# Kernel tuning notes

Hardware: AMD Instinct MI355X
Metric: run time of the kernel (lower is better)

Reference implementation:

```python
import jax, jax.numpy as jnp
import numpy as np

Nx, Nu, Ny, Np, H = 2, 1, 2, 8, 32
Nz = Np * (Nx + Nu)  # 24
B, T = 4096, 256
F, V, Delta = 0.1, 1.0, 1.0  # ps.squeeze(), volume, sample time
ymean = jnp.array([0.5, 0.5], jnp.float32)
ystd = jnp.array([0.3, 0.2], jnp.float32)
umean = jnp.array([1.0], jnp.float32)
ustd = jnp.array([0.5], jnp.float32)


def fnn(x, params):
    # dense layers: tanh hidden, linear output
    for W, b in params[:-1]:
        x = jnp.tanh(x @ W + b)
    W, b = params[-1]
    return x @ W + b


def fxzu(x, z, u, p1, p2, p3):
    # dCa/dt = F*(Caf-Ca)/V - r1 ; dCb/dt = -F*Cb/V + r1 - 3*r2 + r3
    Castd, Cbstd = ystd[0:1], ystd[1:2]
    r1 = fnn(x[:, 0:1], p1) * Castd
    r2 = fnn(x[:, 1:2], p2) * Cbstd
    r3 = fnn(z, p3) * Cbstd
    xs = x * ystd + ymean
    us = u * ustd + umean
    Ca, Cb, Caf = xs[:, 0:1], xs[:, 1:2], us[:, 0:1]
    dCa = F * (Caf - Ca) / V - r1
    dCb = -F * Cb / V + r1 - 3.0 * r2 + r3
    return jnp.concatenate([dCa, dCb], axis=-1) / ystd


def interp(yseq):
    # (B,(Np+1)*Nx) -> (B, Np*Nx): midpoints of consecutive Nx-blocks
    b = yseq.shape[0]
    y = yseq.reshape(b, Np + 1, Nx)
    return (0.5 * (y[:, :-1] + y[:, 1:])).reshape(b, Np * Nx)


def run(useq, xz0, p1, p2, p3):
    def step(xz, u):
        x, z = xz[:, :Nx], xz[:, Nx:]
        xpseq, upseq = z[:, :Np * Nx], z[:, Np * Nx:]
        k1 = fxzu(x, z, u, p1, p2, p3)
        z23 = jnp.concatenate([interp(jnp.concatenate([xpseq, x], -1)), upseq], -1)
        k2 = fxzu(x + Delta * k1 / 2, z23, u, p1, p2, p3)
        k3 = fxzu(x + Delta * k2 / 2, z23, u, p1, p2, p3)
        z4 = jnp.concatenate([xpseq[:, Nx:], x, upseq], -1)
        k4 = fxzu(x + Delta * k3, z4, u, p1, p2, p3)
        xplus = x + (Delta / 6.0) * (k1 + 2 * k2 + 2 * k3 + k4)
        zplus = jnp.concatenate([xpseq[:, Nx:], x, upseq[:, Nu:], u], -1)
        return jnp.concatenate([xplus, zplus], -1), x  # output is pre-update x
    _, ys = jax.lax.scan(step, xz0, jnp.swapaxes(useq, 0, 1))
    return jnp.swapaxes(ys, 0, 1)  # (B, T, Ny)


def setup_inputs() -> dict:
    key = jax.random.key(0)
    ks = jax.random.split(key, 12)
    inp = {
        'useq': jax.random.normal(ks[0], (B, T, Nu), jnp.float32),
        'xz0': jax.random.normal(ks[1], (B, Nx + Nz), jnp.float32),
    }
    dims = {'r1': [1, H, H, 1], 'r2': [1, H, H, 1], 'r3': [Nz, H, H, 1]}
    i = 2
    for name, ds in dims.items():
        for l, (din, dout) in enumerate(zip(ds[:-1], ds[1:])):
            inp[f'{name}W{l}'] = jax.random.normal(ks[i], (din, dout), jnp.float32) / np.sqrt(din).astype(np.float32)
            inp[f'{name}b{l}'] = jnp.zeros((dout,), jnp.float32)
            i += 1
    return inp


def reference(useq, xz0, r1W0, r1b0, r1W1, r1b1, r1W2, r1b2,
              r2W0, r2b0, r2W1, r2b1, r2W2, r2b2,
              r3W0, r3b0, r3W1, r3b1, r3W2, r3b2):
    p1 = [(r1W0, r1b0), (r1W1, r1b1), (r1W2, r1b2)]
    p2 = [(r2W0, r2b0), (r2W1, r2b1), (r2W2, r2b2)]
    p3 = [(r3W0, r3b0), (r3W1, r3b1), (r3W2, r3b2)]
    return run(useq, xz0, p1, p2, p3)
```

## Files before the change

kernel.cpp:

```cpp
#include <hip/hip_runtime.h>

#define DEVINL static __device__ __forceinline__
#define CFENCE() asm volatile("" ::: "memory")

typedef float v2f __attribute__((ext_vector_type(2)));

DEVINL v2f mk2(float a, float b) { v2f r; r.x = a; r.y = b; return r; }
DEVINL v2f pkfma(v2f a, v2f b, v2f c) { return __builtin_elementwise_fma(a, b, c); }

constexpr float KE = 2.885390081777927f;

#if __has_builtin(__builtin_amdgcn_exp2f)
DEVINL float exp2_fast(float x) { return __builtin_amdgcn_exp2f(x); }
#else
DEVINL float exp2_fast(float x) { return __expf(x * 0.6931471805599453f); }
#endif

DEVINL float tanh_pre(float t) {
  float e = exp2_fast(t);
  return 1.0f - 2.0f * __builtin_amdgcn_rcpf(e + 1.0f);
}

template <int CTRL>
DEVINL float dpp_add(float v) {
  int t = __builtin_amdgcn_update_dpp(0, __float_as_int(v), CTRL, 0xF, 0xF, true);
  return v + __int_as_float(t);
}
DEVINL float halves_total(float v) {
  v = dpp_add<0xB1>(v);
  v = dpp_add<0x4E>(v);
  v = dpp_add<0x141>(v);
  v = dpp_add<0x140>(v);
  v = dpp_add<0x142>(v);
  return v;
}
DEVINL float rlane(float v, int l) {
  return __int_as_float(__builtin_amdgcn_readlane(__float_as_int(v), l));
}

DEVINL float dot32(const float* hrow, const v2f* W, float bias) {
  const float4* hp = (const float4*)hrow;
  v2f a0 = mk2(bias, 0.f), a1 = mk2(0.f, 0.f);
  v2f a2 = mk2(0.f, 0.f), a3 = mk2(0.f, 0.f);
#pragma unroll
  for (int q = 0; q < 8; q += 2) {
    float4 x = hp[q], y = hp[q + 1];
    a0 = pkfma(mk2(x.x, x.y), W[2 * q + 0], a0);
    a1 = pkfma(mk2(x.z, x.w), W[2 * q + 1], a1);
    a2 = pkfma(mk2(y.x, y.y), W[2 * q + 2], a2);
    a3 = pkfma(mk2(y.z, y.w), W[2 * q + 3], a3);
  }
  v2f s = (a0 + a1) + (a2 + a3);
  return s.x + s.y;
}
DEVINL float pdot16(const float* hrow, const v2f* W) {
  const float4* hp = (const float4*)hrow;
  v2f a0 = mk2(0.f, 0.f), a1 = mk2(0.f, 0.f);
  float4 x = hp[0], y = hp[1];
  a0 = pkfma(mk2(x.x, x.y), W[0], a0);
  a1 = pkfma(mk2(x.z, x.w), W[1], a1);
  a0 = pkfma(mk2(y.x, y.y), W[2], a0);
  a1 = pkfma(mk2(y.z, y.w), W[3], a1);
  x = hp[2]; y = hp[3];
  a0 = pkfma(mk2(x.x, x.y), W[4], a0);
  a1 = pkfma(mk2(x.z, x.w), W[5], a1);
  a0 = pkfma(mk2(y.x, y.y), W[6], a0);
  a1 = pkfma(mk2(y.z, y.w), W[7], a1);
  v2f s = a0 + a1;
  return s.x + s.y;
}

constexpr int TT = 256;

__global__ __attribute__((amdgpu_flat_work_group_size(64, 64)))
__attribute__((amdgpu_waves_per_eu(4, 4))) void reac_kernel(
    const float* __restrict__ useq,
    const float* __restrict__ xz0,
    const float* __restrict__ r1W0, const float* __restrict__ r1b0,
    const float* __restrict__ r1W1, const float* __restrict__ r1b1,
    const float* __restrict__ r1W2, const float* __restrict__ r1b2,
    const float* __restrict__ r2W0, const float* __restrict__ r2b0,
    const float* __restrict__ r2W1, const float* __restrict__ r2b1,
    const float* __restrict__ r2W2, const float* __restrict__ r2b2,
    const float* __restrict__ r3W0, const float* __restrict__ r3b0,
    const float* __restrict__ r3W1, const float* __restrict__ r3b1,
    const float* __restrict__ r3W2, const float* __restrict__ r3b2,
    float2* __restrict__ out)
{
  const int lane = threadIdx.x;
  const int j = lane & 31;
  const bool hi = lane >= 32;
  const int b = blockIdx.x;
  const int xaddr = ((lane ^ 32) << 2);

  auto xchg = [&](float v) -> float {
    return __int_as_float(__builtin_amdgcn_ds_bpermute(xaddr, __float_as_int(v)));
  };

  const float* W0p = hi ? r2W0 : r1W0;
  const float* B0p = hi ? r2b0 : r1b0;
  const float* W1p = hi ? r2W1 : r1W1;
  const float* B1p = hi ? r2b1 : r1b1;
  const float* W2p = hi ? r2W2 : r1W2;
  const float sc = hi ? 0.2f : 0.3f;
  float w0K = W0p[j] * KE, b0K = B0p[j] * KE;
  float b1K = B1p[j] * KE;
  float w2sc = W2p[j] * sc;

  v2f W1v[16];
#pragma unroll
  for (int k = 0; k < 16; ++k)
    W1v[k] = mk2(W1p[(2 * k) * 32 + j] * KE, W1p[(2 * k + 1) * 32 + j] * KE);

  v2f W0Cv[12];
#pragma unroll
  for (int m = 0; m < 12; ++m)
    W0Cv[m] = mk2(r3W0[(2 * m) * 32 + j] * KE, r3W0[(2 * m + 1) * 32 + j] * KE);
  const int kbase = hi ? 16 : 0;
  v2f W1Cv[8];
#pragma unroll
  for (int k = 0; k < 8; ++k)
    W1Cv[k] = mk2(r3W1[(kbase + 2 * k) * 32 + j] * KE,
                  r3W1[(kbase + 2 * k + 1) * 32 + j] * KE);
  float b0CK = r3b0[j] * KE, b1CK = r3b1[j] * KE;
  float w2C02 = r3W2[j] * 0.2f;

  const float b2sA = r1b2[0] * 0.3f;
  const float b2sB = r2b2[0] * 0.2f;
  const float b2Cs = r3b2[0] * 0.2f - 0.05f;

  __shared__ __align__(16) float zs[24];
  __shared__ __align__(16) float zb[16];
  __shared__ __align__(16) float h12[2][32];
  __shared__ __align__(16) float hR3[3][32];

  float x0 = xz0[b * 26 + 0];
  float x1 = xz0[b * 26 + 1];
  if (!hi && j < 24) zs[j] = xz0[b * 26 + 2 + j];
  CFENCE();

  auto stage = [&](float sxv, float syv, float rc_m05, float CafF,
                   float& kx, float& ky) {
    float sv = hi ? syv : sxv;
    float h = tanh_pre(fmaf(sv, w0K, b0K));
    CFENCE();
    h12[hi][j] = h;
    CFENCE();
    float a = dot32(&h12[hi][0], W1v, b1K);
    float v = halves_total(tanh_pre(a) * w2sc);
    float ra = rlane(v, 31) + b2sA;
    float rb = rlane(v, 63) + b2sB;
    float dCa = fmaf(-0.03f, sxv, CafF) - ra;
    float dCb = fmaf(-0.02f, syv, fmaf(-3.0f, rb, ra) + rc_m05);
    kx = dCa * (1.0f / 0.3f);
    ky = dCb * (1.0f / 0.2f);
  };

  float u = useq[b * TT];

  for (int t = 0; t < TT; ++t) {
    int tn = (t < TT - 1) ? (t + 1) : t;
    float u_nxt = useq[b * TT + tn];
    float CafF = fmaf(u, 0.05f, 0.05f);

    if (lane == 0) out[b * TT + t] = make_float2(x0, x1);

    CFENCE();
    if (!hi && j < 16) {
      zb[j] = (j < 14) ? zs[j + 2] : ((j == 14) ? x0 : x1);
    }
    CFENCE();

    const float4* zp = (const float4*)(hi ? &zb[0] : &zs[0]);
    float4 z0 = zp[0], z1 = zp[1], z2 = zp[2], z3 = zp[3];
    const float4* up = (const float4*)&zs[16];
    float4 u0 = up[0], u1 = up[1];
    v2f aa = mk2(b0CK, 0.f), ab = mk2(0.f, 0.f);
    aa = pkfma(mk2(z0.x, z0.y), W0Cv[0], aa);
    ab = pkfma(mk2(z0.z, z0.w), W0Cv[1], ab);
    aa = pkfma(mk2(z1.x, z1.y), W0Cv[2], aa);
    ab = pkfma(mk2(z1.z, z1.w), W0Cv[3], ab);
    aa = pkfma(mk2(z2.x, z2.y), W0Cv[4], aa);
    ab = pkfma(mk2(z2.z, z2.w), W0Cv[5], ab);
    aa = pkfma(mk2(z3.x, z3.y), W0Cv[6], aa);
    ab = pkfma(mk2(z3.z, z3.w), W0Cv[7], ab);
    aa = pkfma(mk2(u0.x, u0.y), W0Cv[8], aa);
    ab = pkfma(mk2(u0.z, u0.w), W0Cv[9], ab);
    aa = pkfma(mk2(u1.x, u1.y), W0Cv[10], aa);
    ab = pkfma(mk2(u1.z, u1.w), W0Cv[11], ab);
    v2f as = aa + ab;
    float A = as.x + as.y;
    float Ap = xchg(A);
    float tA = tanh_pre(A);
    CFENCE();
    if (!hi) {
      hR3[0][j] = tA;
      hR3[1][j] = tanh_pre(0.5f * (A + Ap));
    } else {
      hR3[2][j] = tA;
    }
    CFENCE();
    float p0 = pdot16(&hR3[0][kbase], W1Cv);
    float p1 = pdot16(&hR3[1][kbase], W1Cv);
    float p2 = pdot16(&hR3[2][kbase], W1Cv);
    float o0 = p0 + xchg(p0) + b1CK;
    float o1 = p1 + xchg(p1) + b1CK;
    float o2 = p2 + xchg(p2) + b1CK;
    float v0 = halves_total(tanh_pre(o0) * w2C02);
    float v1 = halves_total(tanh_pre(o1) * w2C02);
    float v2 = halves_total(tanh_pre(o2) * w2C02);
    float rc1  = rlane(v0, 31) + b2Cs;
    float rc23 = rlane(v1, 31) + b2Cs;
    float rc4  = rlane(v2, 31) + b2Cs;

    float kx1, ky1, kx2, ky2, kx3, ky3, kx4, ky4;
    stage(x0, x1, rc1, CafF, kx1, ky1);
    stage(fmaf(kx1, 0.5f, x0), fmaf(ky1, 0.5f, x1), rc23, CafF, kx2, ky2);
    stage(fmaf(kx2, 0.5f, x0), fmaf(ky2, 0.5f, x1), rc23, CafF, kx3, ky3);
    stage(x0 + kx3, x1 + ky3, rc4, CafF, kx4, ky4);

    float znew = 0.0f;
    bool updz = (!hi) && (j < 24);
    if (updz) znew = (j < 16) ? zb[j] : ((j < 23) ? zs[j + 1] : u);
    CFENCE();
    if (updz) zs[j] = znew;
    x0 += (kx1 + 2.0f * (kx2 + kx3) + kx4) * (1.0f / 6.0f);
    x1 += (ky1 + 2.0f * (ky2 + ky3) + ky4) * (1.0f / 6.0f);
    u = u_nxt;
    CFENCE();
  }
}

extern "C" void kernel_launch(void* const* d_in, const int* in_sizes, int n_in,
                              void* d_out, int out_size, void* d_ws, size_t ws_size,
                              hipStream_t stream) {
  const float* p[20];
  for (int i = 0; i < 20; ++i) p[i] = (const float*)d_in[i];
  reac_kernel<<<dim3(4096), dim3(64), 0, stream>>>(
      p[0], p[1], p[2], p[3], p[4], p[5], p[6], p[7], p[8], p[9], p[10],
      p[11], p[12], p[13], p[14], p[15], p[16], p[17], p[18], p[19],
      (float2*)d_out);
}
```

Before: 850.6 us.

## Software-pipeline r3 network across steps and fold z-shift into weights

Restructures the per-step schedule so the z-dependent part of the r3 first layer and the rc1 evaluation for the next step are computed during the current step's RK stages. The shifted z4 input is handled by permuting the upper-half weights and adding x-dependent terms via a separate weight pair, which removes the zb shared buffer and one layer-two evaluation per step. It also adds a block-index-dependent s_sleep at start to stagger wave phases. The cost is more complex LDS ordering, and it relies on wavefront-level implicit synchronisation between the shared-memory writes and reads.

```diff
diff --git a/kernel.cpp b/kernel.cpp
--- a/kernel.cpp
+++ b/kernel.cpp
@@ -93,6 +93,12 @@
   const int b = blockIdx.x;
   const int xaddr = ((lane ^ 32) << 2);
 
+  {
+    int phase = (b >> 8) & 3;
+    if (phase & 1) __builtin_amdgcn_s_sleep(2);
+    if (phase & 2) __builtin_amdgcn_s_sleep(4);
+  }
+
   auto xchg = [&](float v) -> float {
     return __int_as_float(__builtin_amdgcn_ds_bpermute(xaddr, __float_as_int(v)));
   };
@@ -114,8 +120,14 @@
 
   v2f W0Cv[12];
 #pragma unroll
-  for (int m = 0; m < 12; ++m)
-    W0Cv[m] = mk2(r3W0[(2 * m) * 32 + j] * KE, r3W0[(2 * m + 1) * 32 + j] * KE);
+  for (int m = 0; m < 12; ++m) {
+    int r = (hi && m >= 1 && m <= 7) ? (2 * m - 2) : (2 * m);
+    v2f w = mk2(r3W0[r * 32 + j] * KE, r3W0[(r + 1) * 32 + j] * KE);
+    if (hi && m == 0) w = mk2(0.f, 0.f);
+    W0Cv[m] = w;
+  }
+  const v2f WXv = mk2(r3W0[14 * 32 + j] * KE, r3W0[15 * 32 + j] * KE);
+
   const int kbase = hi ? 16 : 0;
   v2f W1Cv[8];
 #pragma unroll
@@ -130,7 +142,6 @@
   const float b2Cs = r3b2[0] * 0.2f - 0.05f;
 
   __shared__ __align__(16) float zs[24];
-  __shared__ __align__(16) float zb[16];
   __shared__ __align__(16) float h12[2][32];
   __shared__ __align__(16) float hR3[3][32];
 
@@ -139,13 +150,37 @@
   if (!hi && j < 24) zs[j] = xz0[b * 26 + 2 + j];
   CFENCE();
 
-  auto stage = [&](float sxv, float syv, float rc_m05, float CafF,
-                   float& kx, float& ky) {
+  auto r3_l0 = [&](v2f& aaO, v2f& abO) {
+    const float4* zp4 = (const float4*)&zs[0];
+    float4 z0v = zp4[0], z1v = zp4[1], z2v = zp4[2], z3v = zp4[3];
+    float4 u0v = zp4[4], u1v = zp4[5];
+    v2f aa = mk2(b0CK, 0.f), ab = mk2(0.f, 0.f);
+    aa = pkfma(mk2(z0v.x, z0v.y), W0Cv[0], aa);
+    ab = pkfma(mk2(z0v.z, z0v.w), W0Cv[1], ab);
+    aa = pkfma(mk2(z1v.x, z1v.y), W0Cv[2], aa);
+    ab = pkfma(mk2(z1v.z, z1v.w), W0Cv[3], ab);
+    aa = pkfma(mk2(z2v.x, z2v.y), W0Cv[4], aa);
+    ab = pkfma(mk2(z2v.z, z2v.w), W0Cv[5], ab);
+    aa = pkfma(mk2(z3v.x, z3v.y), W0Cv[6], aa);
+    ab = pkfma(mk2(z3v.z, z3v.w), W0Cv[7], ab);
+    aa = pkfma(mk2(u0v.x, u0v.y), W0Cv[8], aa);
+    ab = pkfma(mk2(u0v.z, u0v.w), W0Cv[9], ab);
+    aa = pkfma(mk2(u1v.x, u1v.y), W0Cv[10], aa);
+    ab = pkfma(mk2(u1v.z, u1v.w), W0Cv[11], ab);
+    aaO = aa; abO = ab;
+  };
+  auto rc1_eval = [&]() -> float {
+    float p0 = pdot16(&hR3[0][kbase], W1Cv);
+    float o0 = p0 + xchg(p0) + b1CK;
+    return rlane(halves_total(tanh_pre(o0) * w2C02), 31) + b2Cs;
+  };
+
+  auto net_pre = [&](float sxv, float syv) -> float {
     float sv = hi ? syv : sxv;
-    float h = tanh_pre(fmaf(sv, w0K, b0K));
-    CFENCE();
-    h12[hi][j] = h;
-    CFENCE();
+    return tanh_pre(fmaf(sv, w0K, b0K));
+  };
+  auto net_post = [&](float sxv, float syv, float rc_m05, float CafF,
+                      float& kx, float& ky) {
     float a = dot32(&h12[hi][0], W1v, b1K);
     float v = halves_total(tanh_pre(a) * w2sc);
     float ra = rlane(v, 31) + b2sA;
@@ -156,6 +191,19 @@
     ky = dCb * (1.0f / 0.2f);
   };
 
+  v2f aa4, ab4;
+  float Az;
+  r3_l0(aa4, ab4);
+  {
+    v2f s = aa4 + ab4;
+    Az = s.x + s.y;
+    float h0 = tanh_pre(Az);
+    CFENCE();
+    if (!hi) hR3[0][j] = h0;
+    CFENCE();
+  }
+  float rc1 = rc1_eval();
+
   float u = useq[b * TT];
 
   for (int t = 0; t < TT; ++t) {
@@ -165,65 +213,62 @@
 
     if (lane == 0) out[b * TT + t] = make_float2(x0, x1);
 
-    CFENCE();
-    if (!hi && j < 16) {
-      zb[j] = (j < 14) ? zs[j + 2] : ((j == 14) ? x0 : x1);
-    }
-    CFENCE();
-
-    const float4* zp = (const float4*)(hi ? &zb[0] : &zs[0]);
-    float4 z0 = zp[0], z1 = zp[1], z2 = zp[2], z3 = zp[3];
-    const float4* up = (const float4*)&zs[16];
-    float4 u0 = up[0], u1 = up[1];
-    v2f aa = mk2(b0CK, 0.f), ab = mk2(0.f, 0.f);
-    aa = pkfma(mk2(z0.x, z0.y), W0Cv[0], aa);
-    ab = pkfma(mk2(z0.z, z0.w), W0Cv[1], ab);
-    aa = pkfma(mk2(z1.x, z1.y), W0Cv[2], aa);
-    ab = pkfma(mk2(z1.z, z1.w), W0Cv[3], ab);
-    aa = pkfma(mk2(z2.x, z2.y), W0Cv[4], aa);
-    ab = pkfma(mk2(z2.z, z2.w), W0Cv[5], ab);
-    aa = pkfma(mk2(z3.x, z3.y), W0Cv[6], aa);
-    ab = pkfma(mk2(z3.z, z3.w), W0Cv[7], ab);
-    aa = pkfma(mk2(u0.x, u0.y), W0Cv[8], aa);
-    ab = pkfma(mk2(u0.z, u0.w), W0Cv[9], ab);
-    aa = pkfma(mk2(u1.x, u1.y), W0Cv[10], aa);
-    ab = pkfma(mk2(u1.z, u1.w), W0Cv[11], ab);
-    v2f as = aa + ab;
-    float A = as.x + as.y;
-    float Ap = xchg(A);
-    float tA = tanh_pre(A);
-    CFENCE();
-    if (!hi) {
-      hR3[0][j] = tA;
-      hR3[1][j] = tanh_pre(0.5f * (A + Ap));
-    } else {
-      hR3[2][j] = tA;
-    }
-    CFENCE();
-    float p0 = pdot16(&hR3[0][kbase], W1Cv);
+    ab4 = pkfma(mk2(x0, x1), WXv, ab4);
+    v2f s4v = aa4 + ab4;
+    float A4 = s4v.x + s4v.y;
+    float Apart = xchg(hi ? A4 : Az);
+    float targ = hi ? A4 : (0.5f * (Az + Apart));
+    float hh = tanh_pre(targ);
+    float h1 = net_pre(x0, x1);
+    CFENCE();
+    hR3[1 + hi][j] = hh;
+    h12[hi][j] = h1;
+    CFENCE();
     float p1 = pdot16(&hR3[1][kbase], W1Cv);
     float p2 = pdot16(&hR3[2][kbase], W1Cv);
-    float o0 = p0 + xchg(p0) + b1CK;
     float o1 = p1 + xchg(p1) + b1CK;
     float o2 = p2 + xchg(p2) + b1CK;
-    float v0 = halves_total(tanh_pre(o0) * w2C02);
-    float v1 = halves_total(tanh_pre(o1) * w2C02);
-    float v2 = halves_total(tanh_pre(o2) * w2C02);
-    float rc1  = rlane(v0, 31) + b2Cs;
-    float rc23 = rlane(v1, 31) + b2Cs;
-    float rc4  = rlane(v2, 31) + b2Cs;
-
-    float kx1, ky1, kx2, ky2, kx3, ky3, kx4, ky4;
-    stage(x0, x1, rc1, CafF, kx1, ky1);
-    stage(fmaf(kx1, 0.5f, x0), fmaf(ky1, 0.5f, x1), rc23, CafF, kx2, ky2);
-    stage(fmaf(kx2, 0.5f, x0), fmaf(ky2, 0.5f, x1), rc23, CafF, kx3, ky3);
-    stage(x0 + kx3, x1 + ky3, rc4, CafF, kx4, ky4);
-
-    float znew = 0.0f;
-    bool updz = (!hi) && (j < 24);
-    if (updz) znew = (j < 16) ? zb[j] : ((j < 23) ? zs[j + 1] : u);
-    CFENCE();
-    if (updz) zs[j] = znew;
+    float vv = halves_total(tanh_pre(hi ? o2 : o1) * w2C02);
+    float rc23 = rlane(vv, 31) + b2Cs;
+    float rc4  = rlane(vv, 63) + b2Cs;
+    float kx1, ky1;
+    net_post(x0, x1, rc1, CafF, kx1, ky1);
+    float sx2 = fmaf(kx1, 0.5f, x0), sy2 = fmaf(ky1, 0.5f, x1);
+    float h2 = net_pre(sx2, sy2);
+    CFENCE();
+    h12[hi][j] = h2;
+    CFENCE();
+    float kx2, ky2;
+    net_post(sx2, sy2, rc23, CafF, kx2, ky2);
+    {
+      int src = (j < 14) ? (j + 2) : ((j < 23) ? (j + 1) : 0);
+      float zread = zs[src];
+      float znew = (j == 14) ? x0 : ((j == 15) ? x1 : ((j == 23) ? u : zread));
+      if ((!hi) && (j < 24)) zs[j] = znew;
+    }
+    CFENCE();
+    r3_l0(aa4, ab4);
+    {
+      v2f sv2 = aa4 + ab4;
+      Az = sv2.x + sv2.y;
+      float h0n = tanh_pre(Az);
+      if (!hi) hR3[0][j] = h0n;
+    }
+    float sx3 = fmaf(kx2, 0.5f, x0), sy3 = fmaf(ky2, 0.5f, x1);
+    float h3 = net_pre(sx3, sy3);
+    CFENCE();
+    h12[hi][j] = h3;
+    CFENCE();
+    float kx3, ky3;
+    net_post(sx3, sy3, rc23, CafF, kx3, ky3);
+    rc1 = rc1_eval();
+    float sx4 = x0 + kx3, sy4 = x1 + ky3;
+    float h4 = net_pre(sx4, sy4);
+    CFENCE();
+    h12[hi][j] = h4;
+    CFENCE();
+    float kx4, ky4;
+    net_post(sx4, sy4, rc4, CafF, kx4, ky4);
     x0 += (kx1 + 2.0f * (kx2 + kx3) + kx4) * (1.0f / 6.0f);
     x1 += (ky1 + 2.0f * (ky2 + ky3) + ky4) * (1.0f / 6.0f);
     u = u_nxt;
```

Result: faster. 790.4 us (-7.1%).

## Map one batch element per half-wave and software-pipeline r3 layer-0 across steps

Applied to the files above, without the earlier changes.

Each 32-lane half-wave now handles a whole batch element: it holds both r1 and r2 weights plus the full r3 W1, and grid size is halved. The r3 first layer is split so the x-dependent term is added incrementally. The next step's z-part is computed early, overlapping with stage 3/4, and reductions use a DPP plus ds_swizzle within 32 lanes. This removes cross-half exchanges and readlane broadcasts, at the cost of more registers (waves_per_eu lowered to 2) and more serial work per lane.

```diff
diff --git a/kernel.cpp b/kernel.cpp
--- a/kernel.cpp
+++ b/kernel.cpp
@@ -26,16 +26,13 @@
   int t = __builtin_amdgcn_update_dpp(0, __float_as_int(v), CTRL, 0xF, 0xF, true);
   return v + __int_as_float(t);
 }
-DEVINL float halves_total(float v) {
+DEVINL float elem_total(float v) {
   v = dpp_add<0xB1>(v);
   v = dpp_add<0x4E>(v);
   v = dpp_add<0x141>(v);
   v = dpp_add<0x140>(v);
-  v = dpp_add<0x142>(v);
-  return v;
-}
-DEVINL float rlane(float v, int l) {
-  return __int_as_float(__builtin_amdgcn_readlane(__float_as_int(v), l));
+  int s = __builtin_amdgcn_ds_swizzle(__float_as_int(v), 0x401F);
+  return v + __int_as_float(s);
 }
 
 DEVINL float dot32(const float* hrow, const v2f* W, float bias) {
@@ -53,27 +50,11 @@
   v2f s = (a0 + a1) + (a2 + a3);
   return s.x + s.y;
 }
-DEVINL float pdot16(const float* hrow, const v2f* W) {
-  const float4* hp = (const float4*)hrow;
-  v2f a0 = mk2(0.f, 0.f), a1 = mk2(0.f, 0.f);
-  float4 x = hp[0], y = hp[1];
-  a0 = pkfma(mk2(x.x, x.y), W[0], a0);
-  a1 = pkfma(mk2(x.z, x.w), W[1], a1);
-  a0 = pkfma(mk2(y.x, y.y), W[2], a0);
-  a1 = pkfma(mk2(y.z, y.w), W[3], a1);
-  x = hp[2]; y = hp[3];
-  a0 = pkfma(mk2(x.x, x.y), W[4], a0);
-  a1 = pkfma(mk2(x.z, x.w), W[5], a1);
-  a0 = pkfma(mk2(y.x, y.y), W[6], a0);
-  a1 = pkfma(mk2(y.z, y.w), W[7], a1);
-  v2f s = a0 + a1;
-  return s.x + s.y;
-}
 
 constexpr int TT = 256;
 
 __global__ __attribute__((amdgpu_flat_work_group_size(64, 64)))
-__attribute__((amdgpu_waves_per_eu(4, 4))) void reac_kernel(
+__attribute__((amdgpu_waves_per_eu(2, 2))) void reac_kernel(
     const float* __restrict__ useq,
     const float* __restrict__ xz0,
     const float* __restrict__ r1W0, const float* __restrict__ r1b0,
@@ -91,37 +72,33 @@
   const int j = lane & 31;
   const bool hi = lane >= 32;
   const int b = blockIdx.x;
-  const int xaddr = ((lane ^ 32) << 2);
-
-  auto xchg = [&](float v) -> float {
-    return __int_as_float(__builtin_amdgcn_ds_bpermute(xaddr, __float_as_int(v)));
-  };
-
-  const float* W0p = hi ? r2W0 : r1W0;
-  const float* B0p = hi ? r2b0 : r1b0;
-  const float* W1p = hi ? r2W1 : r1W1;
-  const float* B1p = hi ? r2b1 : r1b1;
-  const float* W2p = hi ? r2W2 : r1W2;
-  const float sc = hi ? 0.2f : 0.3f;
-  float w0K = W0p[j] * KE, b0K = B0p[j] * KE;
-  float b1K = B1p[j] * KE;
-  float w2sc = W2p[j] * sc;
-
-  v2f W1v[16];
+  const int ge = 2 * b + (hi ? 1 : 0);
+
+  float w0K1 = r1W0[j] * KE, b0K1 = r1b0[j] * KE;
+  float w0K2 = r2W0[j] * KE, b0K2 = r2b0[j] * KE;
+  float b1K1 = r1b1[j] * KE, b1K2 = r2b1[j] * KE;
+  float w2s1 = r1W2[j] * 0.3f, w2s2 = r2W2[j] * 0.2f;
+
+  v2f W1a[16], W1b[16];
+#pragma unroll
+  for (int k = 0; k < 16; ++k) {
+    W1a[k] = mk2(r1W1[(2 * k) * 32 + j] * KE, r1W1[(2 * k + 1) * 32 + j] * KE);
+    W1b[k] = mk2(r2W1[(2 * k) * 32 + j] * KE, r2W1[(2 * k + 1) * 32 + j] * KE);
+  }
+
+  v2f WZ[8], WU[4];
+#pragma unroll
+  for (int m = 0; m < 8; ++m)
+    WZ[m] = mk2(r3W0[(2 * m) * 32 + j] * KE, r3W0[(2 * m + 1) * 32 + j] * KE);
+#pragma unroll
+  for (int m = 0; m < 4; ++m)
+    WU[m] = mk2(r3W0[(16 + 2 * m) * 32 + j] * KE,
+                r3W0[(17 + 2 * m) * 32 + j] * KE);
+
+  v2f W1C[16];
 #pragma unroll
   for (int k = 0; k < 16; ++k)
-    W1v[k] = mk2(W1p[(2 * k) * 32 + j] * KE, W1p[(2 * k + 1) * 32 + j] * KE);
-
-  v2f W0Cv[12];
-#pragma unroll
-  for (int m = 0; m < 12; ++m)
-    W0Cv[m] = mk2(r3W0[(2 * m) * 32 + j] * KE, r3W0[(2 * m + 1) * 32 + j] * KE);
-  const int kbase = hi ? 16 : 0;
-  v2f W1Cv[8];
-#pragma unroll
-  for (int k = 0; k < 8; ++k)
-    W1Cv[k] = mk2(r3W1[(kbase + 2 * k) * 32 + j] * KE,
-                  r3W1[(kbase + 2 * k + 1) * 32 + j] * KE);
+    W1C[k] = mk2(r3W1[(2 * k) * 32 + j] * KE, r3W1[(2 * k + 1) * 32 + j] * KE);
   float b0CK = r3b0[j] * KE, b1CK = r3b1[j] * KE;
   float w2C02 = r3W2[j] * 0.2f;
 
@@ -129,103 +106,155 @@
   const float b2sB = r2b2[0] * 0.2f;
   const float b2Cs = r3b2[0] * 0.2f - 0.05f;
 
-  __shared__ __align__(16) float zs[24];
-  __shared__ __align__(16) float zb[16];
-  __shared__ __align__(16) float h12[2][32];
-  __shared__ __align__(16) float hR3[3][32];
-
-  float x0 = xz0[b * 26 + 0];
-  float x1 = xz0[b * 26 + 1];
-  if (!hi && j < 24) zs[j] = xz0[b * 26 + 2 + j];
+  __shared__ __align__(16) float zs2[2][24];
+  __shared__ __align__(16) float h12s[2][2][32];
+  __shared__ __align__(16) float hR3s[2][3][32];
+
+  float* zse  = &zs2[hi ? 1 : 0][0];
+  float* h12a = &h12s[hi ? 1 : 0][0][0];
+  float* h12b = h12a + 32;
+  float* hR3e = &hR3s[hi ? 1 : 0][0][0];
+
+  float x0 = xz0[ge * 26 + 0];
+  float x1 = xz0[ge * 26 + 1];
+  if (j < 24) zse[j] = xz0[ge * 26 + 2 + j];
   CFENCE();
 
-  auto stage = [&](float sxv, float syv, float rc_m05, float CafF,
-                   float& kx, float& ky) {
-    float sv = hi ? syv : sxv;
-    float h = tanh_pre(fmaf(sv, w0K, b0K));
-    CFENCE();
-    h12[hi][j] = h;
-    CFENCE();
-    float a = dot32(&h12[hi][0], W1v, b1K);
-    float v = halves_total(tanh_pre(a) * w2sc);
-    float ra = rlane(v, 31) + b2sA;
-    float rb = rlane(v, 63) + b2sB;
-    float dCa = fmaf(-0.03f, sxv, CafF) - ra;
-    float dCb = fmaf(-0.02f, syv, fmaf(-3.0f, rb, ra) + rc_m05);
+  auto r3_l0 = [&](float& AzO, float& A4pO) {
+    const float4* zp = (const float4*)zse;
+    float4 z0v = zp[0], z1v = zp[1], z2v = zp[2], z3v = zp[3];
+    float4 u0v = zp[4], u1v = zp[5];
+    v2f pa = mk2(b0CK, 0.f), pb = mk2(0.f, 0.f);
+    pa = pkfma(mk2(z0v.x, z0v.y), WZ[0], pa);
+    pb = pkfma(mk2(z0v.z, z0v.w), WZ[1], pb);
+    pa = pkfma(mk2(z1v.x, z1v.y), WZ[2], pa);
+    pb = pkfma(mk2(z1v.z, z1v.w), WZ[3], pb);
+    pa = pkfma(mk2(z2v.x, z2v.y), WZ[4], pa);
+    pb = pkfma(mk2(z2v.z, z2v.w), WZ[5], pb);
+    pa = pkfma(mk2(z3v.x, z3v.y), WZ[6], pa);
+    pb = pkfma(mk2(z3v.z, z3v.w), WZ[7], pb);
+    pa = pkfma(mk2(u0v.x, u0v.y), WU[0], pa);
+    pb = pkfma(mk2(u0v.z, u0v.w), WU[1], pb);
+    pa = pkfma(mk2(u1v.x, u1v.y), WU[2], pa);
+    pb = pkfma(mk2(u1v.z, u1v.w), WU[3], pb);
+    v2f s = pa + pb;
+    AzO = s.x + s.y;
+    v2f qa = mk2(b0CK, 0.f), qb = mk2(0.f, 0.f);
+    qa = pkfma(mk2(z0v.z, z0v.w), WZ[0], qa);
+    qb = pkfma(mk2(z1v.x, z1v.y), WZ[1], qb);
+    qa = pkfma(mk2(z1v.z, z1v.w), WZ[2], qa);
+    qb = pkfma(mk2(z2v.x, z2v.y), WZ[3], qb);
+    qa = pkfma(mk2(z2v.z, z2v.w), WZ[4], qa);
+    qb = pkfma(mk2(z3v.x, z3v.y), WZ[5], qb);
+    qa = pkfma(mk2(z3v.z, z3v.w), WZ[6], qa);
+    qb = pkfma(mk2(u0v.x, u0v.y), WU[0], qb);
+    qa = pkfma(mk2(u0v.z, u0v.w), WU[1], qa);
+    qb = pkfma(mk2(u1v.x, u1v.y), WU[2], qb);
+    qa = pkfma(mk2(u1v.z, u1v.w), WU[3], qa);
+    v2f s2 = qa + qb;
+    A4pO = s2.x + s2.y;
+  };
+
+  auto stage_finish = [&](float a1, float a2, float sx, float sy, float rc,
+                          float CafF, float& kx, float& ky) {
+    float ra = elem_total(tanh_pre(a1) * w2s1) + b2sA;
+    float rb = elem_total(tanh_pre(a2) * w2s2) + b2sB;
+    float dCa = fmaf(-0.03f, sx, CafF) - ra;
+    float dCb = fmaf(-0.02f, sy, fmaf(-3.0f, rb, ra) + rc);
     kx = dCa * (1.0f / 0.3f);
     ky = dCb * (1.0f / 0.2f);
   };
 
-  float u = useq[b * TT];
+  float Az, A4p;
+  r3_l0(Az, A4p);
+  {
+    float h0 = tanh_pre(Az);
+    CFENCE();
+    hR3e[j] = h0;
+    CFENCE();
+  }
+  float o0 = dot32(hR3e, W1C, b1CK);
+  float rc1 = elem_total(tanh_pre(o0) * w2C02) + b2Cs;
+
+  const float* up = useq + ge * TT;
+  float2* outp = out + ge * TT;
+  float u = up[0];
 
   for (int t = 0; t < TT; ++t) {
     int tn = (t < TT - 1) ? (t + 1) : t;
-    float u_nxt = useq[b * TT + tn];
+    float u_nxt = up[tn];
     float CafF = fmaf(u, 0.05f, 0.05f);
 
-    if (lane == 0) out[b * TT + t] = make_float2(x0, x1);
-
-    CFENCE();
-    if (!hi && j < 16) {
-      zb[j] = (j < 14) ? zs[j + 2] : ((j == 14) ? x0 : x1);
-    }
-    CFENCE();
-
-    const float4* zp = (const float4*)(hi ? &zb[0] : &zs[0]);
-    float4 z0 = zp[0], z1 = zp[1], z2 = zp[2], z3 = zp[3];
-    const float4* up = (const float4*)&zs[16];
-    float4 u0 = up[0], u1 = up[1];
-    v2f aa = mk2(b0CK, 0.f), ab = mk2(0.f, 0.f);
-    aa = pkfma(mk2(z0.x, z0.y), W0Cv[0], aa);
-    ab = pkfma(mk2(z0.z, z0.w), W0Cv[1], ab);
-    aa = pkfma(mk2(z1.x, z1.y), W0Cv[2], aa);
-    ab = pkfma(mk2(z1.z, z1.w), W0Cv[3], ab);
-    aa = pkfma(mk2(z2.x, z2.y), W0Cv[4], aa);
-    ab = pkfma(mk2(z2.z, z2.w), W0Cv[5], ab);
-    aa = pkfma(mk2(z3.x, z3.y), W0Cv[6], aa);
-    ab = pkfma(mk2(z3.z, z3.w), W0Cv[7], ab);
-    aa = pkfma(mk2(u0.x, u0.y), W0Cv[8], aa);
-    ab = pkfma(mk2(u0.z, u0.w), W0Cv[9], ab);
-    aa = pkfma(mk2(u1.x, u1.y), W0Cv[10], aa);
-    ab = pkfma(mk2(u1.z, u1.w), W0Cv[11], ab);
-    v2f as = aa + ab;
-    float A = as.x + as.y;
-    float Ap = xchg(A);
-    float tA = tanh_pre(A);
-    CFENCE();
-    if (!hi) {
-      hR3[0][j] = tA;
-      hR3[1][j] = tanh_pre(0.5f * (A + Ap));
-    } else {
-      hR3[2][j] = tA;
-    }
-    CFENCE();
-    float p0 = pdot16(&hR3[0][kbase], W1Cv);
-    float p1 = pdot16(&hR3[1][kbase], W1Cv);
-    float p2 = pdot16(&hR3[2][kbase], W1Cv);
-    float o0 = p0 + xchg(p0) + b1CK;
-    float o1 = p1 + xchg(p1) + b1CK;
-    float o2 = p2 + xchg(p2) + b1CK;
-    float v0 = halves_total(tanh_pre(o0) * w2C02);
-    float v1 = halves_total(tanh_pre(o1) * w2C02);
-    float v2 = halves_total(tanh_pre(o2) * w2C02);
-    float rc1  = rlane(v0, 31) + b2Cs;
-    float rc23 = rlane(v1, 31) + b2Cs;
-    float rc4  = rlane(v2, 31) + b2Cs;
-
-    float kx1, ky1, kx2, ky2, kx3, ky3, kx4, ky4;
-    stage(x0, x1, rc1, CafF, kx1, ky1);
-    stage(fmaf(kx1, 0.5f, x0), fmaf(ky1, 0.5f, x1), rc23, CafF, kx2, ky2);
-    stage(fmaf(kx2, 0.5f, x0), fmaf(ky2, 0.5f, x1), rc23, CafF, kx3, ky3);
-    stage(x0 + kx3, x1 + ky3, rc4, CafF, kx4, ky4);
-
-    float znew = 0.0f;
-    bool updz = (!hi) && (j < 24);
-    if (updz) znew = (j < 16) ? zb[j] : ((j < 23) ? zs[j + 1] : u);
-    CFENCE();
-    if (updz) zs[j] = znew;
+    if (j == 0) outp[t] = make_float2(x0, x1);
+
+    float A4 = fmaf(x1, WZ[7].y, fmaf(x0, WZ[7].x, A4p));
+    float A23 = 0.5f * (Az + A4);
+    float h23 = tanh_pre(A23);
+    float h4v = tanh_pre(A4);
+    float g1a = tanh_pre(fmaf(x0, w0K1, b0K1));
+    float g1b = tanh_pre(fmaf(x1, w0K2, b0K2));
+    CFENCE();
+    hR3e[32 + j] = h23;
+    hR3e[64 + j] = h4v;
+    h12a[j] = g1a;
+    h12b[j] = g1b;
+    CFENCE();
+    float o1 = dot32(hR3e + 32, W1C, b1CK);
+    float o2 = dot32(hR3e + 64, W1C, b1CK);
+    float a1 = dot32(h12a, W1a, b1K1);
+    float a2 = dot32(h12b, W1b, b1K2);
+    float rc23 = elem_total(tanh_pre(o1) * w2C02) + b2Cs;
+    float rc4  = elem_total(tanh_pre(o2) * w2C02) + b2Cs;
+    float kx1, ky1;
+    stage_finish(a1, a2, x0, x1, rc1, CafF, kx1, ky1);
+    float sx2 = fmaf(kx1, 0.5f, x0), sy2 = fmaf(ky1, 0.5f, x1);
+    float g2a = tanh_pre(fmaf(sx2, w0K1, b0K1));
+    float g2b = tanh_pre(fmaf(sy2, w0K2, b0K2));
+    CFENCE();
+    h12a[j] = g2a;
+    h12b[j] = g2b;
+    CFENCE();
+    float a1_2 = dot32(h12a, W1a, b1K1);
+    float a2_2 = dot32(h12b, W1b, b1K2);
+    int src = (j < 14) ? (j + 2) : ((j < 23) ? (j + 1) : 0);
+    float zread = zse[src];
+    float kx2, ky2;
+    stage_finish(a1_2, a2_2, sx2, sy2, rc23, CafF, kx2, ky2);
+    float znew = (j == 14) ? x0 : ((j == 15) ? x1 : ((j == 23) ? u : zread));
+    CFENCE();
+    if (j < 24) zse[j] = znew;
+    float sx3 = fmaf(kx2, 0.5f, x0), sy3 = fmaf(ky2, 0.5f, x1);
+    float g3a = tanh_pre(fmaf(sx3, w0K1, b0K1));
+    float g3b = tanh_pre(fmaf(sy3, w0K2, b0K2));
+    CFENCE();
+    h12a[j] = g3a;
+    h12b[j] = g3b;
+    CFENCE();
+    float a1_3 = dot32(h12a, W1a, b1K1);
+    float a2_3 = dot32(h12b, W1b, b1K2);
+    float Azn, A4pn;
+    r3_l0(Azn, A4pn);
+    float kx3, ky3;
+    stage_finish(a1_3, a2_3, sx3, sy3, rc23, CafF, kx3, ky3);
+    float sx4 = x0 + kx3, sy4 = x1 + ky3;
+    float g4a = tanh_pre(fmaf(sx4, w0K1, b0K1));
+    float g4b = tanh_pre(fmaf(sy4, w0K2, b0K2));
+    float h0n = tanh_pre(Azn);
+    CFENCE();
+    h12a[j] = g4a;
+    h12b[j] = g4b;
+    hR3e[j] = h0n;
+    CFENCE();
+    float a1_4 = dot32(h12a, W1a, b1K1);
+    float a2_4 = dot32(h12b, W1b, b1K2);
+    float o0n = dot32(hR3e, W1C, b1CK);
+    float kx4, ky4;
+    stage_finish(a1_4, a2_4, sx4, sy4, rc4, CafF, kx4, ky4);
+    rc1 = elem_total(tanh_pre(o0n) * w2C02) + b2Cs;
     x0 += (kx1 + 2.0f * (kx2 + kx3) + kx4) * (1.0f / 6.0f);
     x1 += (ky1 + 2.0f * (ky2 + ky3) + ky4) * (1.0f / 6.0f);
+    Az = Azn;
+    A4p = A4pn;
     u = u_nxt;
     CFENCE();
   }
@@ -236,7 +265,7 @@
                               hipStream_t stream) {
   const float* p[20];
   for (int i = 0; i < 20; ++i) p[i] = (const float*)d_in[i];
-  reac_kernel<<<dim3(4096), dim3(64), 0, stream>>>(
+  reac_kernel<<<dim3(2048), dim3(64), 0, stream>>>(
       p[0], p[1], p[2], p[3], p[4], p[5], p[6], p[7], p[8], p[9], p[10],
       p[11], p[12], p[13], p[14], p[15], p[16], p[17], p[18], p[19],
       (float2*)d_out);
```

Measured after the change: 803.6 us. -5.5%, faster.

## Process two batch elements per wave with interleaved, software-pipelined RK4 stages

Applied to the files above, without the earlier changes.

Each 64-lane wave now handles two batch rows, interleaving their independent dependency chains to expose more instruction-level parallelism in the latency-bound serial scan. The r3 first layer is restructured so the z4 variant reuses partial accumulators plus an x-only update, and the next step's rc1 network is computed early, overlapping with stage 3. The DPP reduction is shortened to 16-lane groups combined via readlane. Grid halves and waves_per_eu drops to 2, trading occupancy for more registers and ILP.

```diff
diff --git a/kernel.cpp b/kernel.cpp
--- a/kernel.cpp
+++ b/kernel.cpp
@@ -26,16 +26,15 @@
   int t = __builtin_amdgcn_update_dpp(0, __float_as_int(v), CTRL, 0xF, 0xF, true);
   return v + __int_as_float(t);
 }
-DEVINL float halves_total(float v) {
+DEVINL float rlane(float v, int l) {
+  return __int_as_float(__builtin_amdgcn_readlane(__float_as_int(v), l));
+}
+DEVINL float psum4(float v) {
   v = dpp_add<0xB1>(v);
   v = dpp_add<0x4E>(v);
   v = dpp_add<0x141>(v);
   v = dpp_add<0x140>(v);
-  v = dpp_add<0x142>(v);
   return v;
-}
-DEVINL float rlane(float v, int l) {
-  return __int_as_float(__builtin_amdgcn_readlane(__float_as_int(v), l));
 }
 
 DEVINL float dot32(const float* hrow, const v2f* W, float bias) {
@@ -73,7 +72,7 @@
 constexpr int TT = 256;
 
 __global__ __attribute__((amdgpu_flat_work_group_size(64, 64)))
-__attribute__((amdgpu_waves_per_eu(4, 4))) void reac_kernel(
+__attribute__((amdgpu_waves_per_eu(2, 2))) void reac_kernel(
     const float* __restrict__ useq,
     const float* __restrict__ xz0,
     const float* __restrict__ r1W0, const float* __restrict__ r1b0,
@@ -114,8 +113,14 @@
 
   v2f W0Cv[12];
 #pragma unroll
-  for (int m = 0; m < 12; ++m)
-    W0Cv[m] = mk2(r3W0[(2 * m) * 32 + j] * KE, r3W0[(2 * m + 1) * 32 + j] * KE);
+  for (int m = 0; m < 12; ++m) {
+    int r = (hi && m >= 1 && m <= 7) ? (2 * m - 2) : (2 * m);
+    v2f w = mk2(r3W0[r * 32 + j] * KE, r3W0[(r + 1) * 32 + j] * KE);
+    if (hi && m == 0) w = mk2(0.f, 0.f);
+    W0Cv[m] = w;
+  }
+  v2f WXv = mk2(r3W0[14 * 32 + j] * KE, r3W0[15 * 32 + j] * KE);
+
   const int kbase = hi ? 16 : 0;
   v2f W1Cv[8];
 #pragma unroll
@@ -129,52 +134,31 @@
   const float b2sB = r2b2[0] * 0.2f;
   const float b2Cs = r3b2[0] * 0.2f - 0.05f;
 
-  __shared__ __align__(16) float zs[24];
-  __shared__ __align__(16) float zb[16];
-  __shared__ __align__(16) float h12[2][32];
-  __shared__ __align__(16) float hR3[3][32];
-
-  float x0 = xz0[b * 26 + 0];
-  float x1 = xz0[b * 26 + 1];
-  if (!hi && j < 24) zs[j] = xz0[b * 26 + 2 + j];
+  __shared__ __align__(16) float zsS[2][24];
+  __shared__ __align__(16) float h12S[2][2][32];
+  __shared__ __align__(16) float hR3S[2][3][32];
+
+  struct Elem {
+    float x0, x1, Az, rc1, u;
+    v2f aa4, ab4;
+    float* zs; float* h12; float* hR3;
+    const float* up; float2* outp;
+  } EA, EB;
+  EA.zs = &zsS[0][0]; EA.h12 = &h12S[0][0][0]; EA.hR3 = &hR3S[0][0][0];
+  EB.zs = &zsS[1][0]; EB.h12 = &h12S[1][0][0]; EB.hR3 = &hR3S[1][0][0];
+  EA.up = useq + (2 * b + 0) * TT; EA.outp = out + (2 * b + 0) * TT;
+  EB.up = useq + (2 * b + 1) * TT; EB.outp = out + (2 * b + 1) * TT;
+
+  EA.x0 = xz0[(2 * b + 0) * 26 + 0]; EA.x1 = xz0[(2 * b + 0) * 26 + 1];
+  EB.x0 = xz0[(2 * b + 1) * 26 + 0]; EB.x1 = xz0[(2 * b + 1) * 26 + 1];
+  if (!hi && j < 24) EA.zs[j] = xz0[(2 * b + 0) * 26 + 2 + j];
+  if (hi && j < 24)  EB.zs[j] = xz0[(2 * b + 1) * 26 + 2 + j];
   CFENCE();
 
-  auto stage = [&](float sxv, float syv, float rc_m05, float CafF,
-                   float& kx, float& ky) {
-    float sv = hi ? syv : sxv;
-    float h = tanh_pre(fmaf(sv, w0K, b0K));
-    CFENCE();
-    h12[hi][j] = h;
-    CFENCE();
-    float a = dot32(&h12[hi][0], W1v, b1K);
-    float v = halves_total(tanh_pre(a) * w2sc);
-    float ra = rlane(v, 31) + b2sA;
-    float rb = rlane(v, 63) + b2sB;
-    float dCa = fmaf(-0.03f, sxv, CafF) - ra;
-    float dCb = fmaf(-0.02f, syv, fmaf(-3.0f, rb, ra) + rc_m05);
-    kx = dCa * (1.0f / 0.3f);
-    ky = dCb * (1.0f / 0.2f);
-  };
-
-  float u = useq[b * TT];
-
-  for (int t = 0; t < TT; ++t) {
-    int tn = (t < TT - 1) ? (t + 1) : t;
-    float u_nxt = useq[b * TT + tn];
-    float CafF = fmaf(u, 0.05f, 0.05f);
-
-    if (lane == 0) out[b * TT + t] = make_float2(x0, x1);
-
-    CFENCE();
-    if (!hi && j < 16) {
-      zb[j] = (j < 14) ? zs[j + 2] : ((j == 14) ? x0 : x1);
-    }
-    CFENCE();
-
-    const float4* zp = (const float4*)(hi ? &zb[0] : &zs[0]);
+  auto r3_l0 = [&](Elem& E) {
+    const float4* zp = (const float4*)E.zs;
     float4 z0 = zp[0], z1 = zp[1], z2 = zp[2], z3 = zp[3];
-    const float4* up = (const float4*)&zs[16];
-    float4 u0 = up[0], u1 = up[1];
+    float4 u0 = zp[4], u1 = zp[5];
     v2f aa = mk2(b0CK, 0.f), ab = mk2(0.f, 0.f);
     aa = pkfma(mk2(z0.x, z0.y), W0Cv[0], aa);
     ab = pkfma(mk2(z0.z, z0.w), W0Cv[1], ab);
@@ -188,45 +172,152 @@
     ab = pkfma(mk2(u0.z, u0.w), W0Cv[9], ab);
     aa = pkfma(mk2(u1.x, u1.y), W0Cv[10], aa);
     ab = pkfma(mk2(u1.z, u1.w), W0Cv[11], ab);
-    v2f as = aa + ab;
-    float A = as.x + as.y;
-    float Ap = xchg(A);
-    float tA = tanh_pre(A);
-    CFENCE();
-    if (!hi) {
-      hR3[0][j] = tA;
-      hR3[1][j] = tanh_pre(0.5f * (A + Ap));
-    } else {
-      hR3[2][j] = tA;
+    E.aa4 = aa; E.ab4 = ab;
+    v2f s = aa + ab;
+    E.Az = s.x + s.y;
+  };
+  auto rc1_eval = [&](Elem& E) -> float {
+    float p0 = pdot16(&E.hR3[kbase], W1Cv);
+    float o0 = p0 + xchg(p0) + b1CK;
+    float v = psum4(tanh_pre(o0) * w2C02);
+    return (rlane(v, 15) + rlane(v, 31)) + b2Cs;
+  };
+  auto net_pre = [&](float sxv, float syv) -> float {
+    float sv = hi ? syv : sxv;
+    return tanh_pre(fmaf(sv, w0K, b0K));
+  };
+  auto net_post = [&](Elem& E, float sxv, float syv, float rc_m05,
+                      float CafF, float& kx, float& ky) {
+    float a = dot32(&E.h12[hi ? 32 : 0], W1v, b1K);
+    float v = psum4(tanh_pre(a) * w2sc);
+    float ra = (rlane(v, 15) + rlane(v, 31)) + b2sA;
+    float rb = (rlane(v, 47) + rlane(v, 63)) + b2sB;
+    float dCa = fmaf(-0.03f, sxv, CafF) - ra;
+    float dCb = fmaf(-0.02f, syv, fmaf(-3.0f, rb, ra) + rc_m05);
+    kx = dCa * (1.0f / 0.3f);
+    ky = dCb * (1.0f / 0.2f);
+  };
+
+  r3_l0(EA);
+  r3_l0(EB);
+  {
+    float h0A = tanh_pre(EA.Az);
+    float h0B = tanh_pre(EB.Az);
+    CFENCE();
+    if (!hi) { EA.hR3[j] = h0A; EB.hR3[j] = h0B; }
+    CFENCE();
+  }
+  EA.rc1 = rc1_eval(EA);
+  EB.rc1 = rc1_eval(EB);
+  EA.u = EA.up[0];
+  EB.u = EB.up[0];
+
+  for (int t = 0; t < TT; ++t) {
+    int tn = (t < TT - 1) ? (t + 1) : t;
+    float uAn = EA.up[tn], uBn = EB.up[tn];
+    float CafFA = fmaf(EA.u, 0.05f, 0.05f);
+    float CafFB = fmaf(EB.u, 0.05f, 0.05f);
+
+    {
+      float2 val = hi ? make_float2(EB.x0, EB.x1) : make_float2(EA.x0, EA.x1);
+      float2* addr = hi ? EB.outp : EA.outp;
+      if (j == 0) addr[t] = val;
     }
-    CFENCE();
-    float p0 = pdot16(&hR3[0][kbase], W1Cv);
-    float p1 = pdot16(&hR3[1][kbase], W1Cv);
-    float p2 = pdot16(&hR3[2][kbase], W1Cv);
-    float o0 = p0 + xchg(p0) + b1CK;
-    float o1 = p1 + xchg(p1) + b1CK;
-    float o2 = p2 + xchg(p2) + b1CK;
-    float v0 = halves_total(tanh_pre(o0) * w2C02);
-    float v1 = halves_total(tanh_pre(o1) * w2C02);
-    float v2 = halves_total(tanh_pre(o2) * w2C02);
-    float rc1  = rlane(v0, 31) + b2Cs;
-    float rc23 = rlane(v1, 31) + b2Cs;
-    float rc4  = rlane(v2, 31) + b2Cs;
-
-    float kx1, ky1, kx2, ky2, kx3, ky3, kx4, ky4;
-    stage(x0, x1, rc1, CafF, kx1, ky1);
-    stage(fmaf(kx1, 0.5f, x0), fmaf(ky1, 0.5f, x1), rc23, CafF, kx2, ky2);
-    stage(fmaf(kx2, 0.5f, x0), fmaf(ky2, 0.5f, x1), rc23, CafF, kx3, ky3);
-    stage(x0 + kx3, x1 + ky3, rc4, CafF, kx4, ky4);
-
-    float znew = 0.0f;
-    bool updz = (!hi) && (j < 24);
-    if (updz) znew = (j < 16) ? zb[j] : ((j < 23) ? zs[j + 1] : u);
-    CFENCE();
-    if (updz) zs[j] = znew;
-    x0 += (kx1 + 2.0f * (kx2 + kx3) + kx4) * (1.0f / 6.0f);
-    x1 += (ky1 + 2.0f * (ky2 + ky3) + ky4) * (1.0f / 6.0f);
-    u = u_nxt;
+
+    EA.ab4 = pkfma(mk2(EA.x0, EA.x1), WXv, EA.ab4);
+    EB.ab4 = pkfma(mk2(EB.x0, EB.x1), WXv, EB.ab4);
+    v2f s4A = EA.aa4 + EA.ab4;
+    v2f s4B = EB.aa4 + EB.ab4;
+    float A4A = s4A.x + s4A.y;
+    float A4B = s4B.x + s4B.y;
+    float ApA = xchg(hi ? A4A : EA.Az);
+    float ApB = xchg(hi ? A4B : EB.Az);
+    float tgA = hi ? A4A : (0.5f * (EA.Az + ApA));
+    float tgB = hi ? A4B : (0.5f * (EB.Az + ApB));
+    float hhA = tanh_pre(tgA);
+    float hhB = tanh_pre(tgB);
+    float h1A = net_pre(EA.x0, EA.x1);
+    float h1B = net_pre(EB.x0, EB.x1);
+    CFENCE();
+    EA.hR3[32 * (1 + (hi ? 1 : 0)) + j] = hhA;
+    EB.hR3[32 * (1 + (hi ? 1 : 0)) + j] = hhB;
+    EA.h12[(hi ? 32 : 0) + j] = h1A;
+    EB.h12[(hi ? 32 : 0) + j] = h1B;
+    CFENCE();
+    float p1A = pdot16(&EA.hR3[32 + kbase], W1Cv);
+    float p2A = pdot16(&EA.hR3[64 + kbase], W1Cv);
+    float p1B = pdot16(&EB.hR3[32 + kbase], W1Cv);
+    float p2B = pdot16(&EB.hR3[64 + kbase], W1Cv);
+    float o1A = p1A + xchg(p1A) + b1CK;
+    float o2A = p2A + xchg(p2A) + b1CK;
+    float o1B = p1B + xchg(p1B) + b1CK;
+    float o2B = p2B + xchg(p2B) + b1CK;
+    float vvA = psum4(tanh_pre(hi ? o2A : o1A) * w2C02);
+    float vvB = psum4(tanh_pre(hi ? o2B : o1B) * w2C02);
+    float rc23A = (rlane(vvA, 15) + rlane(vvA, 31)) + b2Cs;
+    float rc4A  = (rlane(vvA, 47) + rlane(vvA, 63)) + b2Cs;
+    float rc23B = (rlane(vvB, 15) + rlane(vvB, 31)) + b2Cs;
+    float rc4B  = (rlane(vvB, 47) + rlane(vvB, 63)) + b2Cs;
+    float kx1A, ky1A, kx1B, ky1B;
+    net_post(EA, EA.x0, EA.x1, EA.rc1, CafFA, kx1A, ky1A);
+    net_post(EB, EB.x0, EB.x1, EB.rc1, CafFB, kx1B, ky1B);
+    float sx2A = fmaf(kx1A, 0.5f, EA.x0), sy2A = fmaf(ky1A, 0.5f, EA.x1);
+    float sx2B = fmaf(kx1B, 0.5f, EB.x0), sy2B = fmaf(ky1B, 0.5f, EB.x1);
+    float h2A = net_pre(sx2A, sy2A);
+    float h2B = net_pre(sx2B, sy2B);
+    CFENCE();
+    EA.h12[(hi ? 32 : 0) + j] = h2A;
+    EB.h12[(hi ? 32 : 0) + j] = h2B;
+    CFENCE();
+    float kx2A, ky2A, kx2B, ky2B;
+    net_post(EA, sx2A, sy2A, rc23A, CafFA, kx2A, ky2A);
+    net_post(EB, sx2B, sy2B, rc23B, CafFB, kx2B, ky2B);
+    int src = (j < 14) ? (j + 2) : ((j < 23) ? (j + 1) : 0);
+    float zrA = EA.zs[src];
+    float zrB = EB.zs[src];
+    float znA = (j == 14) ? EA.x0
+              : ((j == 15) ? EA.x1 : ((j == 23) ? EA.u : zrA));
+    float znB = (j == 14) ? EB.x0
+              : ((j == 15) ? EB.x1 : ((j == 23) ? EB.u : zrB));
+    CFENCE();
+    if (!hi && j < 24) EA.zs[j] = znA;
+    if (hi && j < 24)  EB.zs[j] = znB;
+    float sx3A = fmaf(kx2A, 0.5f, EA.x0), sy3A = fmaf(ky2A, 0.5f, EA.x1);
+    float sx3B = fmaf(kx2B, 0.5f, EB.x0), sy3B = fmaf(ky2B, 0.5f, EB.x1);
+    float h3A = net_pre(sx3A, sy3A);
+    float h3B = net_pre(sx3B, sy3B);
+    CFENCE();
+    r3_l0(EA);
+    r3_l0(EB);
+    float h0nA = tanh_pre(EA.Az);
+    float h0nB = tanh_pre(EB.Az);
+    if (!hi) { EA.hR3[j] = h0nA; EB.hR3[j] = h0nB; }
+    CFENCE();
+    EA.h12[(hi ? 32 : 0) + j] = h3A;
+    EB.h12[(hi ? 32 : 0) + j] = h3B;
+    CFENCE();
+    float kx3A, ky3A, kx3B, ky3B;
+    net_post(EA, sx3A, sy3A, rc23A, CafFA, kx3A, ky3A);
+    net_post(EB, sx3B, sy3B, rc23B, CafFB, kx3B, ky3B);
+    float rc1An = rc1_eval(EA);
+    float rc1Bn = rc1_eval(EB);
+    float sx4A = EA.x0 + kx3A, sy4A = EA.x1 + ky3A;
+    float sx4B = EB.x0 + kx3B, sy4B = EB.x1 + ky3B;
+    float h4A = net_pre(sx4A, sy4A);
+    float h4B = net_pre(sx4B, sy4B);
+    CFENCE();
+    EA.h12[(hi ? 32 : 0) + j] = h4A;
+    EB.h12[(hi ? 32 : 0) + j] = h4B;
+    CFENCE();
+    float kx4A, ky4A, kx4B, ky4B;
+    net_post(EA, sx4A, sy4A, rc4A, CafFA, kx4A, ky4A);
+    net_post(EB, sx4B, sy4B, rc4B, CafFB, kx4B, ky4B);
+    EA.x0 += (kx1A + 2.0f * (kx2A + kx3A) + kx4A) * (1.0f / 6.0f);
+    EA.x1 += (ky1A + 2.0f * (ky2A + ky3A) + ky4A) * (1.0f / 6.0f);
+    EB.x0 += (kx1B + 2.0f * (kx2B + kx3B) + kx4B) * (1.0f / 6.0f);
+    EB.x1 += (ky1B + 2.0f * (ky2B + ky3B) + ky4B) * (1.0f / 6.0f);
+    EA.rc1 = rc1An; EB.rc1 = rc1Bn;
+    EA.u = uAn; EB.u = uBn;
     CFENCE();
   }
 }
@@ -236,7 +327,7 @@
                               hipStream_t stream) {
   const float* p[20];
   for (int i = 0; i < 20; ++i) p[i] = (const float*)d_in[i];
-  reac_kernel<<<dim3(4096), dim3(64), 0, stream>>>(
+  reac_kernel<<<dim3(2048), dim3(64), 0, stream>>>(
       p[0], p[1], p[2], p[3], p[4], p[5], p[6], p[7], p[8], p[9], p[10],
       p[11], p[12], p[13], p[14], p[15], p[16], p[17], p[18], p[19],
       (float2*)d_out);
```

New measurement: 956.3 us. 12.4% more time.
